# Performance work log

Measured on AMD Instinct MI355X. Metric: run time of the kernel, lower is better.

The kernel has to match this reference:

```python
import jax, jax.numpy as jnp
import numpy as np

DIM = 256
HEADS = 8
HEAD_DIM = DIM // HEADS  # 32
LN_EPS = 1e-5


def setup_inputs() -> dict:
    key = jax.random.key(0)
    ks = jax.random.split(key, 11)
    B, N = 8, 4096
    s = 1.0 / np.sqrt(DIM)
    return {
        "q": jax.random.normal(ks[0], (B, N, DIM), dtype=jnp.float32),
        "k": jax.random.normal(ks[1], (B, N, DIM), dtype=jnp.float32),
        "v": jax.random.normal(ks[2], (B, N, DIM), dtype=jnp.float32),
        "Wq": jax.random.normal(ks[3], (DIM, DIM), dtype=jnp.float32) * s,
        "bq": jax.random.normal(ks[4], (DIM,), dtype=jnp.float32) * 0.01,
        "Wk": jax.random.normal(ks[5], (DIM, DIM), dtype=jnp.float32) * s,
        "bk": jax.random.normal(ks[6], (DIM,), dtype=jnp.float32) * 0.01,
        "Wv": jax.random.normal(ks[7], (DIM, DIM), dtype=jnp.float32) * s,
        "bv": jax.random.normal(ks[8], (DIM,), dtype=jnp.float32) * 0.01,
        "ln_gamma": jnp.ones((DIM,), dtype=jnp.float32),
        "ln_beta": jnp.zeros((DIM,), dtype=jnp.float32),
    }


def _heads(x, B, N):
    # [B, N, DIM] -> [B, HEADS, N, HEAD_DIM]
    return x.reshape(B, N, HEADS, HEAD_DIM).transpose(0, 2, 1, 3)


def reference(q, k, v, Wq, bq, Wk, bk, Wv, bv, ln_gamma, ln_beta):
    B, N, _ = q.shape
    ql = _heads(q @ Wq.T + bq, B, N)
    kl = _heads(k @ Wk.T + bk, B, N)
    vl = _heads(v @ Wv.T + bv, B, N)

    # FFT-domain "attention": rfft2 over (seq, head_dim), complex multiply, irfft2
    q_fft = jnp.fft.rfft2(ql.astype(jnp.float32))   # [B, H, N, HEAD_DIM//2+1] complex
    k_fft = jnp.fft.rfft2(kl.astype(jnp.float32))
    attention = jnp.fft.irfft2(q_fft * k_fft)        # [B, H, N, HEAD_DIM]
    attention = jax.nn.softmax(attention, axis=-1)

    out = vl * attention                             # elementwise value gate
    out = out.transpose(0, 2, 1, 3).reshape(B, N, HEADS * HEAD_DIM)

    # dropout is identity at eval; residual + LayerNorm(256)
    out = out + v
    mu = jnp.mean(out, axis=-1, keepdims=True)
    var = jnp.var(out, axis=-1, keepdims=True)
    out = (out - mu) * jax.lax.rsqrt(var + LN_EPS) * ln_gamma + ln_beta
    return out
```

## Files before the change

### kernel.cpp

```cpp
#include <hip/hip_runtime.h>

#define NFREQ 2049

using cf = float2;
typedef __attribute__((ext_vector_type(8))) short short8;
typedef __attribute__((ext_vector_type(4))) float floatx4;

__device__ inline unsigned short bf16_rne(float x) {
  unsigned u = __float_as_uint(x);
  unsigned r = u + 0x7FFFu + ((u >> 16) & 1u);
  return (unsigned short)(r >> 16);
}
__device__ inline float bf16_to_f(unsigned short h) {
  return __uint_as_float(((unsigned)h) << 16);
}

__global__ __launch_bounds__(256, 4) void gemm_proj(
    const float* __restrict__ X, const float* __restrict__ W,
    const float* __restrict__ bias, float* __restrict__ dst, int mode)
{
  __shared__ __align__(16) unsigned short sm[12416];
  unsigned short* sAhi = sm;
  unsigned short* sAlo = sm + 4128;
  unsigned short* sBhi = sm + 8256;
  unsigned short* sBlo = sm + 10336;

  const int tid = threadIdx.x;
  const int m0 = blockIdx.x * 128;
  const int j0 = blockIdx.y * 64;
  const int wave = tid >> 6, lane = tid & 63;
  const int wm = wave & 1, wj = wave >> 1;
  const int lm = lane & 15, quad = lane >> 4;

  floatx4 acc[4][2] = {};

  for (int k0 = 0; k0 < 256; k0 += 32) {
    float4 xa[4], wb[2];
    #pragma unroll
    for (int r = 0; r < 4; r++) {
      int v = tid + r * 256;
      int row = v >> 3, c4 = (v & 7) * 4;
      xa[r] = *(const float4*)(X + (size_t)(m0 + row) * 256 + k0 + c4);
    }
    #pragma unroll
    for (int r = 0; r < 2; r++) {
      int v = tid + r * 256;
      int row = v >> 3, c4 = (v & 7) * 4;
      wb[r] = *(const float4*)(W + (size_t)(j0 + row) * 256 + k0 + c4);
    }
    __syncthreads();
    #pragma unroll
    for (int r = 0; r < 4; r++) {
      int v = tid + r * 256;
      int row = v >> 3, c4 = (v & 7) * 4;
      int q = c4 >> 3, off = c4 & 7;
      float f[4] = {xa[r].x, xa[r].y, xa[r].z, xa[r].w};
      unsigned short h[4], l[4];
      #pragma unroll
      for (int i = 0; i < 4; i++) {
        h[i] = bf16_rne(f[i]);
        l[i] = bf16_rne(f[i] - bf16_to_f(h[i]));
      }
      int idx = ((q * 129 + row) << 3) + off;
      *(uint2*)&sAhi[idx] = make_uint2((unsigned)h[0] | ((unsigned)h[1] << 16),
                                       (unsigned)h[2] | ((unsigned)h[3] << 16));
      *(uint2*)&sAlo[idx] = make_uint2((unsigned)l[0] | ((unsigned)l[1] << 16),
                                       (unsigned)l[2] | ((unsigned)l[3] << 16));
    }
    #pragma unroll
    for (int r = 0; r < 2; r++) {
      int v = tid + r * 256;
      int row = v >> 3, c4 = (v & 7) * 4;
      int q = c4 >> 3, off = c4 & 7;
      float f[4] = {wb[r].x, wb[r].y, wb[r].z, wb[r].w};
      unsigned short h[4], l[4];
      #pragma unroll
      for (int i = 0; i < 4; i++) {
        h[i] = bf16_rne(f[i]);
        l[i] = bf16_rne(f[i] - bf16_to_f(h[i]));
      }
      int idx = ((q * 65 + row) << 3) + off;
      *(uint2*)&sBhi[idx] = make_uint2((unsigned)h[0] | ((unsigned)h[1] << 16),
                                       (unsigned)h[2] | ((unsigned)h[3] << 16));
      *(uint2*)&sBlo[idx] = make_uint2((unsigned)l[0] | ((unsigned)l[1] << 16),
                                       (unsigned)l[2] | ((unsigned)l[3] << 16));
    }
    __syncthreads();

    short8 ahi[4], alo[4], bhi[2], blo[2];
    #pragma unroll
    for (int mf = 0; mf < 4; mf++) {
      int row = wm * 64 + mf * 16 + lm;
      int idx = ((quad * 129 + row) << 3);
      ahi[mf] = *(const short8*)&sAhi[idx];
      alo[mf] = *(const short8*)&sAlo[idx];
    }
    #pragma unroll
    for (int jf = 0; jf < 2; jf++) {
      int row = wj * 32 + jf * 16 + lm;
      int idx = ((quad * 65 + row) << 3);
      bhi[jf] = *(const short8*)&sBhi[idx];
      blo[jf] = *(const short8*)&sBlo[idx];
    }
    #pragma unroll
    for (int mf = 0; mf < 4; mf++)
      #pragma unroll
      for (int jf = 0; jf < 2; jf++) {
        acc[mf][jf] = __builtin_amdgcn_mfma_f32_16x16x32_bf16(
            ahi[mf], bhi[jf], acc[mf][jf], 0, 0, 0);
        acc[mf][jf] = __builtin_amdgcn_mfma_f32_16x16x32_bf16(
            ahi[mf], blo[jf], acc[mf][jf], 0, 0, 0);
        acc[mf][jf] = __builtin_amdgcn_mfma_f32_16x16x32_bf16(
            alo[mf], bhi[jf], acc[mf][jf], 0, 0, 0);
      }
  }

  #pragma unroll
  for (int jf = 0; jf < 2; jf++) {
    float bj = bias[j0 + wj * 32 + jf * 16 + lm];
    #pragma unroll
    for (int mf = 0; mf < 4; mf++)
      #pragma unroll
      for (int r = 0; r < 4; r++)
        acc[mf][jf][r] += bj;
  }

  if (mode == 2) {
    #pragma unroll
    for (int mf = 0; mf < 4; mf++)
      #pragma unroll
      for (int jf = 0; jf < 2; jf++) {
        int j = j0 + wj * 32 + jf * 16 + lm;
        int mb = m0 + wm * 64 + mf * 16 + quad * 4;
        #pragma unroll
        for (int r = 0; r < 4; r++)
          dst[(size_t)(mb + r) * 256 + j] = acc[mf][jf][r];
      }
  } else {
    const int b = m0 >> 12;
    const int n0 = m0 & 4095;
    #pragma unroll
    for (int mf = 0; mf < 4; mf++)
      #pragma unroll
      for (int jf = 0; jf < 2; jf++) {
        int j = j0 + wj * 32 + jf * 16 + lm;
        int nb = n0 + wm * 64 + mf * 16 + quad * 4;
        float4 o = make_float4(acc[mf][jf][0], acc[mf][jf][1],
                               acc[mf][jf][2], acc[mf][jf][3]);
        *(float4*)(dst + (size_t)(b * 256 + j) * 4096 + nb) = o;
      }
  }
}

#define FFT_LDS 4368

__device__ inline int swz(int i) { return i + (i >> 4) + (i >> 8); }
__device__ inline int digrev4(int n) {
  int b = __brev((unsigned)n) >> 20;
  return ((b & 0x555) << 1) | ((b & 0xAAA) >> 1);
}

template<int SIGN>
__device__ inline void fft4_stages(cf* X, int tid)
{
  #pragma unroll
  for (int s = 0; s < 6; s++) {
    const int q = 1 << (2 * s);
    __syncthreads();
    #pragma unroll
    for (int r = 0; r < 4; r++) {
      int t = tid + r * 256;
      int j = t & (q - 1);
      int base = ((t >> (2 * s)) << (2 * s + 2)) + j;
      cf a = X[swz(base)];
      cf b = X[swz(base + q)];
      cf c = X[swz(base + 2 * q)];
      cf d = X[swz(base + 3 * q)];
      float th = (float)SIGN * 6.283185307179586f * (float)j / (float)(4 * q);
      float s1, c1, s2, c2, s3, c3;
      __sincosf(th, &s1, &c1);
      __sincosf(2.0f * th, &s2, &c2);
      __sincosf(3.0f * th, &s3, &c3);
      cf bt = make_float2(c1 * b.x - s1 * b.y, c1 * b.y + s1 * b.x);
      cf ct = make_float2(c2 * c.x - s2 * c.y, c2 * c.y + s2 * c.x);
      cf dt = make_float2(c3 * d.x - s3 * d.y, c3 * d.y + s3 * d.x);
      cf e0 = make_float2(a.x + ct.x, a.y + ct.y);
      cf e1 = make_float2(a.x - ct.x, a.y - ct.y);
      cf o0 = make_float2(bt.x + dt.x, bt.y + dt.y);
      cf o1 = make_float2(bt.x - dt.x, bt.y - dt.y);
      cf io1 = make_float2(-o1.y, o1.x);
      X[swz(base)]         = make_float2(e0.x + o0.x, e0.y + o0.y);
      X[swz(base + 2 * q)] = make_float2(e0.x - o0.x, e0.y - o0.y);
      if (SIGN < 0) {
        X[swz(base + q)]     = make_float2(e1.x - io1.x, e1.y - io1.y);
        X[swz(base + 3 * q)] = make_float2(e1.x + io1.x, e1.y + io1.y);
      } else {
        X[swz(base + q)]     = make_float2(e1.x + io1.x, e1.y + io1.y);
        X[swz(base + 3 * q)] = make_float2(e1.x - io1.x, e1.y - io1.y);
      }
    }
  }
  __syncthreads();
}

__global__ __launch_bounds__(256) void fft_fwd(
    const float* __restrict__ src_base, cf* __restrict__ dst_base)
{
  __shared__ cf X[FFT_LDS];
  const int c0 = blockIdx.x * 2;
  const float* s0 = src_base + (size_t)c0 * 4096;
  const float* s1 = s0 + 4096;
  const int tid = threadIdx.x;
  #pragma unroll
  for (int i = 0; i < 16; i++) {
    int n = tid + i * 256;
    X[swz(digrev4(n))] = make_float2(s0[n], s1[n]);
  }
  fft4_stages<-1>(X, tid);
  cf* d0 = dst_base + (size_t)c0 * NFREQ;
  cf* d1 = d0 + NFREQ;
  for (int f = tid; f <= 2048; f += 256) {
    cf Zf = X[swz(f)];
    cf Zm = X[swz((4096 - f) & 4095)];
    d0[f] = make_float2(0.5f * (Zf.x + Zm.x), 0.5f * (Zf.y - Zm.y));
    d1[f] = make_float2(0.5f * (Zf.y + Zm.y), 0.5f * (Zm.x - Zf.x));
  }
}

__global__ __launch_bounds__(256, 2) void freq_conv(
    cf* Qf, const cf* __restrict__ Kf)
{
  const int f = blockIdx.x * 256 + threadIdx.x;
  const int bh = blockIdx.y;
  if (f > 2048) return;
  const size_t base = (size_t)bh * 32 * NFREQ + f;
  cf q[32], k[32];
  #pragma unroll
  for (int e = 0; e < 32; e++) {
    q[e] = Qf[base + (size_t)e * NFREQ];
    k[e] = Kf[base + (size_t)e * NFREQ];
  }
  #pragma unroll
  for (int d = 0; d < 32; d++) {
    float ax = 0.0f, ay = 0.0f;
    #pragma unroll
    for (int e = 0; e < 32; e++) {
      cf a = q[e];
      cf b = k[(d - e) & 31];
      ax += a.x * b.x - a.y * b.y;
      ay += a.x * b.y + a.y * b.x;
    }
    Qf[base + (size_t)d * NFREQ] = make_float2(ax, ay);
  }
}

__global__ __launch_bounds__(256) void fft_inv(
    const cf* __restrict__ Cf, float* __restrict__ attn)
{
  __shared__ cf X[FFT_LDS];
  const int c0 = blockIdx.x * 2;
  const cf* s0 = Cf + (size_t)c0 * NFREQ;
  const cf* s1 = s0 + NFREQ;
  const int tid = threadIdx.x;
  for (int f = tid; f <= 2048; f += 256) {
    cf c1 = s0[f];
    cf c2 = s1[f];
    X[swz(digrev4(f))] = make_float2(c1.x - c2.y, c1.y + c2.x);
    if (f != 0 && f != 2048)
      X[swz(digrev4(4096 - f))] = make_float2(c1.x + c2.y, c2.x - c1.y);
  }
  fft4_stages<+1>(X, tid);
  float* d0 = attn + (size_t)c0 * 4096;
  float* d1 = d0 + 4096;
  const float inv = 1.0f / 4096.0f;
  #pragma unroll
  for (int i = 0; i < 16; i++) {
    int n = tid + i * 256;
    cf z = X[swz(n)];
    d0[n] = z.x * inv;
    d1[n] = z.y * inv;
  }
}

__global__ __launch_bounds__(256) void finalize_kernel(
    const float* __restrict__ attn, const float* __restrict__ VL,
    const float* __restrict__ vin, const float* __restrict__ gamma,
    const float* __restrict__ beta, float* __restrict__ out)
{
  __shared__ float At[256][33];
  const int n0 = blockIdx.x * 32;
  const int b = blockIdx.y;
  const int tid = threadIdx.x;
  #pragma unroll
  for (int i = 0; i < 32; i++) {
    int v = tid + i * 256;
    int hd = v >> 5, nn = v & 31;
    At[hd][nn] = attn[(size_t)(b * 256 + hd) * 4096 + n0 + nn];
  }
  __syncthreads();
  const int wave = tid >> 6, lane = tid & 63;
  float g[4], bt[4];
  #pragma unroll
  for (int r = 0; r < 4; r++) { g[r] = gamma[64 * r + lane]; bt[r] = beta[64 * r + lane]; }

  for (int t = 0; t < 8; t++) {
    const int nn = wave * 8 + t;
    const int n = n0 + nn;
    float p[4];
    #pragma unroll
    for (int r = 0; r < 4; r++) {
      float a = At[64 * r + lane][nn];
      float mx = a;
      #pragma unroll
      for (int off = 16; off >= 1; off >>= 1) mx = fmaxf(mx, __shfl_xor(mx, off, 32));
      float e = __expf(a - mx);
      float s = e;
      #pragma unroll
      for (int off = 16; off >= 1; off >>= 1) s += __shfl_xor(s, off, 32);
      p[r] = e / s;
    }
    const size_t base = ((size_t)b * 4096 + n) * 256 + lane;
    float o[4];
    float s1 = 0.0f, s2 = 0.0f;
    #pragma unroll
    for (int r = 0; r < 4; r++) {
      o[r] = VL[base + 64 * r] * p[r] + vin[base + 64 * r];
      s1 += o[r];
      s2 += o[r] * o[r];
    }
    #pragma unroll
    for (int off = 32; off >= 1; off >>= 1) {
      s1 += __shfl_xor(s1, off, 64);
      s2 += __shfl_xor(s2, off, 64);
    }
    float mu = s1 * (1.0f / 256.0f);
    float var = s2 * (1.0f / 256.0f) - mu * mu;
    float rs = rsqrtf(var + 1e-5f);
    #pragma unroll
    for (int r = 0; r < 4; r++)
      out[base + 64 * r] = (o[r] - mu) * rs * g[r] + bt[r];
  }
}

extern "C" void kernel_launch(void* const* d_in, const int* in_sizes, int n_in,
                              void* d_out, int out_size, void* d_ws, size_t ws_size,
                              hipStream_t stream)
{
  const float* q  = (const float*)d_in[0];
  const float* k  = (const float*)d_in[1];
  const float* v  = (const float*)d_in[2];
  const float* Wq = (const float*)d_in[3];
  const float* bq = (const float*)d_in[4];
  const float* Wk = (const float*)d_in[5];
  const float* bk = (const float*)d_in[6];
  const float* Wv = (const float*)d_in[7];
  const float* bv = (const float*)d_in[8];
  const float* ln_gamma = (const float*)d_in[9];
  const float* ln_beta  = (const float*)d_in[10];
  float* out = (float*)d_out;

  float* ws = (float*)d_ws;
  float* QL = ws;
  float* KL = QL + (size_t)8388608;
  float* VL = KL + (size_t)8388608;
  cf* Qf = (cf*)(VL + (size_t)8388608);
  cf* Kf = Qf + (size_t)2048 * NFREQ;
  float* attn = QL;

  gemm_proj<<<dim3(256, 4), 256, 0, stream>>>(q, Wq, bq, QL, 0);
  gemm_proj<<<dim3(256, 4), 256, 0, stream>>>(k, Wk, bk, KL, 1);
  gemm_proj<<<dim3(256, 4), 256, 0, stream>>>(v, Wv, bv, VL, 2);

  fft_fwd<<<1024, 256, 0, stream>>>(QL, Qf);
  fft_fwd<<<1024, 256, 0, stream>>>(KL, Kf);

  freq_conv<<<dim3(9, 64), 256, 0, stream>>>(Qf, Kf);

  fft_inv<<<1024, 256, 0, stream>>>(Qf, attn);

  finalize_kernel<<<dim3(128, 8), 256, 0, stream>>>(attn, VL, v, ln_gamma,
                                                    ln_beta, out);
}
```

Baseline: 319.8 us.

## Replace direct 32-point circular convolution with wave-shuffle FFT in freq_conv

The per-frequency circular convolution over head_dim was computed directly as a 32x32 complex multiply-accumulate per thread. It is now done by a 32-point FFT, a pointwise product and an inverse FFT, with butterflies exchanged across lanes through __shfl_xor. Tiles of 64 frequencies are staged through LDS so that global loads and stores stay coalesced. This cuts arithmetic from O(32^2) to O(32 log 32) per frequency and gives more blocks. The cost is fast sincos twiddles and many cross-lane shuffles, which may add small rounding differences.

```diff
diff --git a/kernel.cpp b/kernel.cpp
--- a/kernel.cpp
+++ b/kernel.cpp
@@ -227,30 +227,100 @@
   }
 }
 
-__global__ __launch_bounds__(256, 2) void freq_conv(
-    cf* Qf, const cf* __restrict__ Kf)
-{
-  const int f = blockIdx.x * 256 + threadIdx.x;
+__device__ inline cf cmul(cf a, cf b) {
+  return make_float2(a.x * b.x - a.y * b.y, a.x * b.y + a.y * b.x);
+}
+
+__device__ inline cf tw_f(int l, int h) {
+  int j = l & (h - 1);
+  if (l & h) {
+    float sn, cs;
+    __sincosf(-3.14159265358979f * (float)j / (float)h, &sn, &cs);
+    return make_float2(cs, sn);
+  }
+  return make_float2(1.0f, 0.0f);
+}
+
+template<int H>
+__device__ inline cf fwd_stage(cf x, cf w, float sg) {
+  float px = __shfl_xor(x.x, H);
+  float py = __shfl_xor(x.y, H);
+  return cmul(make_float2(px + sg * x.x, py + sg * x.y), w);
+}
+template<int H>
+__device__ inline cf inv_stage(cf x, cf w, float sg) {
+  cf t = cmul(x, w);
+  float px = __shfl_xor(t.x, H);
+  float py = __shfl_xor(t.y, H);
+  return make_float2(px + sg * t.x, py + sg * t.y);
+}
+template<int H>
+__device__ inline cf nt_stage(cf x, float sg) {
+  float px = __shfl_xor(x.x, H);
+  float py = __shfl_xor(x.y, H);
+  return make_float2(px + sg * x.x, py + sg * x.y);
+}
+
+__global__ __launch_bounds__(256) void freq_conv(
+    cf* __restrict__ Qf, const cf* __restrict__ Kf)
+{
+  __shared__ cf Qs[32][65];
+  __shared__ cf Ks[32][65];
+  const int f0 = blockIdx.x * 64;
   const int bh = blockIdx.y;
-  if (f > 2048) return;
-  const size_t base = (size_t)bh * 32 * NFREQ + f;
-  cf q[32], k[32];
-  #pragma unroll
-  for (int e = 0; e < 32; e++) {
-    q[e] = Qf[base + (size_t)e * NFREQ];
-    k[e] = Kf[base + (size_t)e * NFREQ];
-  }
-  #pragma unroll
-  for (int d = 0; d < 32; d++) {
-    float ax = 0.0f, ay = 0.0f;
-    #pragma unroll
-    for (int e = 0; e < 32; e++) {
-      cf a = q[e];
-      cf b = k[(d - e) & 31];
-      ax += a.x * b.x - a.y * b.y;
-      ay += a.x * b.y + a.y * b.x;
-    }
-    Qf[base + (size_t)d * NFREQ] = make_float2(ax, ay);
+  const int tid = threadIdx.x;
+  const int wave = tid >> 6, lane = tid & 63;
+  const int d = lane & 31, hl = lane >> 5;
+
+  #pragma unroll
+  for (int i = 0; i < 8; i++) {
+    int v = tid + i * 256;
+    int e = v >> 6, fl = v & 63;
+    int f = f0 + fl;
+    if (f < NFREQ) {
+      Qs[e][fl] = Qf[(size_t)(bh * 32 + e) * NFREQ + f];
+      Ks[e][fl] = Kf[(size_t)(bh * 32 + e) * NFREQ + f];
+    } else {
+      Qs[e][fl] = make_float2(0.0f, 0.0f);
+      Ks[e][fl] = make_float2(0.0f, 0.0f);
+    }
+  }
+  __syncthreads();
+
+  const cf w16 = tw_f(d, 16), w8 = tw_f(d, 8), w4 = tw_f(d, 4), w2 = tw_f(d, 2);
+  const float s16 = (d & 16) ? -1.0f : 1.0f;
+  const float s8  = (d & 8)  ? -1.0f : 1.0f;
+  const float s4  = (d & 4)  ? -1.0f : 1.0f;
+  const float s2  = (d & 2)  ? -1.0f : 1.0f;
+  const float s1  = (d & 1)  ? -1.0f : 1.0f;
+
+  #pragma unroll
+  for (int it = 0; it < 8; it++) {
+    const int fl = it * 8 + wave * 2 + hl;
+    cf q = Qs[d][fl];
+    cf k = Ks[d][fl];
+    q = fwd_stage<16>(q, w16, s16);  k = fwd_stage<16>(k, w16, s16);
+    q = fwd_stage<8>(q, w8, s8);     k = fwd_stage<8>(k, w8, s8);
+    q = fwd_stage<4>(q, w4, s4);     k = fwd_stage<4>(k, w4, s4);
+    q = fwd_stage<2>(q, w2, s2);     k = fwd_stage<2>(k, w2, s2);
+    q = nt_stage<1>(q, s1);          k = nt_stage<1>(k, s1);
+    cf c = cmul(q, k);
+    c = nt_stage<1>(c, s1);
+    c = inv_stage<2>(c, make_float2(w2.x, -w2.y), s2);
+    c = inv_stage<4>(c, make_float2(w4.x, -w4.y), s4);
+    c = inv_stage<8>(c, make_float2(w8.x, -w8.y), s8);
+    c = inv_stage<16>(c, make_float2(w16.x, -w16.y), s16);
+    Qs[d][fl] = make_float2(c.x * (1.0f / 32.0f), c.y * (1.0f / 32.0f));
+  }
+  __syncthreads();
+
+  #pragma unroll
+  for (int i = 0; i < 8; i++) {
+    int v = tid + i * 256;
+    int e = v >> 6, fl = v & 63;
+    int f = f0 + fl;
+    if (f < NFREQ)
+      Qf[(size_t)(bh * 32 + e) * NFREQ + f] = Qs[e][fl];
   }
 }
 
@@ -374,7 +444,7 @@
   fft_fwd<<<1024, 256, 0, stream>>>(QL, Qf);
   fft_fwd<<<1024, 256, 0, stream>>>(KL, Kf);
 
-  freq_conv<<<dim3(9, 64), 256, 0, stream>>>(Qf, Kf);
+  freq_conv<<<dim3(33, 64), 256, 0, stream>>>(Qf, Kf);
 
   fft_inv<<<1024, 256, 0, stream>>>(Qf, attn);
 
```

After: 325.1 us. No clear change (+1.7%).
